# Kernel tuning notes

Hardware: AMD Instinct MI355X
Metric: run time of the kernel (lower is better)

The kernel has to match this reference:

```python
import jax, jax.numpy as jnp
import numpy as np

NAMES = ['tempo', 'chord', 'barbeat', 'type', 'pitch', 'duration', 'velocity']
VOCABS = [56, 135, 18, 4, 87, 18, 25]
EMBS = [128, 256, 64, 32, 512, 128, 128]
B, S, D, H, L, FF = 2, 2048, 512, 8, 8, 2048
HD = D // H
EPS = 1e-6


def _layernorm(x, g, b):
    m = x.mean(-1, keepdims=True)
    v = ((x - m) ** 2).mean(-1, keepdims=True)
    return (x - m) / jnp.sqrt(v + 1e-5) * g + b


def _rope(x, cos, sin):
    x1, x2 = jnp.split(x, 2, -1)
    return x * cos + jnp.concatenate([-x2, x1], -1) * sin


def _causal_linear_attn(q, k, v):
    # kernelized causal linear attention: phi = elu + 1, cumulative-sum normalization
    q = jax.nn.elu(q) + 1.0
    k = jax.nn.elu(k) + 1.0
    kv = jnp.cumsum(jnp.einsum('bshd,bshm->bshdm', k, v), axis=1)  # [B,S,H,HD,HD]
    z = 1.0 / (jnp.einsum('bshd,bshd->bsh', q, jnp.cumsum(k, axis=1)) + EPS)
    return jnp.einsum('bshd,bshdm->bshm', q, kv) * z[..., None]


def _forward(inputs, target, emb_tables, in_W, in_b, Wq, bq, Wk, bk, Wv, bv, Wo, bo,
             ln1_g, ln1_b, ln2_g, ln2_b, W1, b1, W2, b2, norm_g, norm_b, pWs, pbs, catW, catb):
    # multi-field embedding, each scaled by sqrt(d_emb) (CPEmbedding)
    embs = [emb_tables[i][inputs[..., i]] * jnp.sqrt(jnp.float32(EMBS[i])) for i in range(7)]
    x = jnp.concatenate(embs, -1) @ in_W + in_b  # [B,S,D]
    # PositionalEncoding: original indexes pe at position seq_len -> single d_model vector
    div = jnp.exp(jnp.arange(0, D, 2, dtype=jnp.float32) * (-np.log(10000.0) / D))
    pe = jnp.zeros((D,), jnp.float32).at[0::2].set(jnp.sin(S * div)).at[1::2].set(jnp.cos(S * div))
    x = x + pe
    # rotary tables for head_dim
    inv_freq = 1.0 / (10000.0 ** (jnp.arange(0, HD, 2, dtype=jnp.float32) / HD))
    fr = jnp.arange(S, dtype=jnp.float32)[:, None] * inv_freq[None, :]
    ang = jnp.concatenate([fr, fr], -1)  # [S,HD]
    cos = jnp.cos(ang)[None, :, None, :]
    sin = jnp.sin(ang)[None, :, None, :]
    for l in range(L):
        q = (x @ Wq[l] + bq[l]).reshape(B, S, H, HD)
        k = (x @ Wk[l] + bk[l]).reshape(B, S, H, HD)
        v = (x @ Wv[l] + bv[l]).reshape(B, S, H, HD)
        q = _rope(q, cos, sin)
        k = _rope(k, cos, sin)
        a = _causal_linear_attn(q, k, v).reshape(B, S, D) @ Wo[l] + bo[l]
        x = x + a
        y = x = _layernorm(x, ln1_g[l], ln1_b[l])
        y = jax.nn.gelu(y @ W1[l] + b1[l], approximate=False) @ W2[l] + b2[l]
        x = _layernorm(x + y, ln2_g[l], ln2_b[l])
    x = _layernorm(x, norm_g, norm_b)
    # MultiProj with teacher-forced type embedding (target branch)
    emb_t = emb_tables[3][target[..., 3]] * jnp.sqrt(jnp.float32(EMBS[3]))
    proj_type = (x @ pWs[3] + pbs[3]) * jnp.sqrt(jnp.float32(VOCABS[3]))  # from pre-concat x
    xc = jnp.concatenate([x, emb_t], -1) @ catW + catb
    outs = []
    for i in range(7):
        if i == 3:
            outs.append(proj_type)
        else:
            outs.append((xc @ pWs[i] + pbs[i]) * jnp.sqrt(jnp.float32(VOCABS[i])))
    return jnp.concatenate(outs, -1)  # [B,S,sum(VOCABS)=343]


def setup_inputs():
    key = jax.random.key(0)
    kit = iter(jax.random.split(key, 64))
    s = 0.02
    d = {}
    d['inputs'] = jax.random.randint(next(kit), (B, S, 7), 0, 4)
    d['target'] = jax.random.randint(next(kit), (B, S, 7), 0, 4)
    for i, n in enumerate(NAMES):
        d['emb_' + n] = jax.random.normal(next(kit), (VOCABS[i], EMBS[i]), jnp.float32) * s
    E = sum(EMBS)
    d['in_W'] = jax.random.normal(next(kit), (E, D)) * s
    d['in_b'] = jnp.zeros((D,))
    for nm, sh in [('Wq', (L, D, D)), ('Wk', (L, D, D)), ('Wv', (L, D, D)), ('Wo', (L, D, D)), ('W1', (L, D, FF)), ('W2', (L, FF, D))]:
        d[nm] = jax.random.normal(next(kit), sh) * s
    for nm, sh in [('bq', (L, D)), ('bk', (L, D)), ('bv', (L, D)), ('bo', (L, D)), ('b1', (L, FF)), ('b2', (L, D)), ('ln1_b', (L, D)), ('ln2_b', (L, D)), ('norm_b', (D,)), ('catb', (D,))]:
        d[nm] = jnp.zeros(sh)
    d['ln1_g'] = jnp.ones((L, D))
    d['ln2_g'] = jnp.ones((L, D))
    d['norm_g'] = jnp.ones((D,))
    for i, n in enumerate(NAMES):
        d['pW_' + n] = jax.random.normal(next(kit), (D, VOCABS[i])) * s
        d['pb_' + n] = jnp.zeros((VOCABS[i],))
    d['catW'] = jax.random.normal(next(kit), (D + 32, D)) * s
    return d


def reference(inputs, target, emb_tempo, emb_chord, emb_barbeat, emb_type, emb_pitch, emb_duration, emb_velocity,
              in_W, in_b, Wq, bq, Wk, bk, Wv, bv, Wo, bo, ln1_g, ln1_b, ln2_g, ln2_b, W1, b1, W2, b2,
              norm_g, norm_b, pW_tempo, pb_tempo, pW_chord, pb_chord, pW_barbeat, pb_barbeat, pW_type, pb_type,
              pW_pitch, pb_pitch, pW_duration, pb_duration, pW_velocity, pb_velocity, catW, catb):
    emb_tables = [emb_tempo, emb_chord, emb_barbeat, emb_type, emb_pitch, emb_duration, emb_velocity]
    pWs = [pW_tempo, pW_chord, pW_barbeat, pW_type, pW_pitch, pW_duration, pW_velocity]
    pbs = [pb_tempo, pb_chord, pb_barbeat, pb_type, pb_pitch, pb_duration, pb_velocity]
    return _forward(inputs, target, emb_tables, in_W, in_b, Wq, bq, Wk, bk, Wv, bv, Wo, bo,
                    ln1_g, ln1_b, ln2_g, ln2_b, W1, b1, W2, b2, norm_g, norm_b, pWs, pbs, catW, catb)
```

## Files before the change

### kernel.cpp

```cpp
#include <hip/hip_runtime.h>
#include <math.h>

typedef unsigned short u16;
typedef short bf16x8 __attribute__((ext_vector_type(8)));
typedef float f32x4 __attribute__((ext_vector_type(4)));
typedef u16 u16x4 __attribute__((ext_vector_type(4)));
typedef u16 u16x8 __attribute__((ext_vector_type(8)));

#define NB 2
#define NS 2048
#define ND 512
#define NH 8
#define NHD 64
#define NL 8
#define NFF 2048
#define NM (NB*NS)
#define NE 1248
#define NEP 1280
#define NXC 576
#define CHK 64
#define NCH (NS/CHK)
#define QKVW 1536

__device__ inline float b2f(u16 u){ union{ unsigned int i; float f;} x; x.i = ((unsigned int)u)<<16; return x.f; }
__device__ inline u16 f2b(float f){ union{ float f; unsigned int i;} x; x.f=f; unsigned int r = x.i + 0x7fffu + ((x.i>>16)&1u); return (u16)(r>>16); }

__global__ void k_tables(float* rc, float* rs, float* pe){
  int tid = blockIdx.x*blockDim.x + threadIdx.x;
  if (tid < NS*32){
    int s = tid >> 5, j = tid & 31;
    double inv = exp(-(double)(2*j) * log(10000.0) / (double)NHD);
    double ang = (double)s * inv;
    rc[tid] = (float)cos(ang);
    rs[tid] = (float)sin(ang);
  }
  if (tid < ND/2){
    double div = exp(-(double)(2*tid) * log(10000.0) / (double)ND);
    double ang = (double)NS * div;
    pe[2*tid]   = (float)sin(ang);
    pe[2*tid+1] = (float)cos(ang);
  }
}

__global__ void k_embed(const int* __restrict__ inp,
    const float* __restrict__ e0, const float* __restrict__ e1, const float* __restrict__ e2,
    const float* __restrict__ e3, const float* __restrict__ e4, const float* __restrict__ e5,
    const float* __restrict__ e6, u16* __restrict__ xe)
{
  int row = blockIdx.x;
  int i0 = inp[row*7+0], i1 = inp[row*7+1], i2 = inp[row*7+2], i3 = inp[row*7+3],
      i4 = inp[row*7+4], i5 = inp[row*7+5], i6 = inp[row*7+6];
  size_t base = (size_t)row*NEP;
  for (int c = threadIdx.x; c < NEP; c += 256){
    float val = 0.f;
    if      (c < 128)  val = e0[i0*128 + c]        * 11.3137084990f;
    else if (c < 384)  val = e1[i1*256 + (c-128)]  * 16.0f;
    else if (c < 448)  val = e2[i2*64  + (c-384)]  * 8.0f;
    else if (c < 480)  val = e3[i3*32  + (c-448)]  * 5.6568542495f;
    else if (c < 992)  val = e4[i4*512 + (c-480)]  * 22.6274169980f;
    else if (c < 1120) val = e5[i5*128 + (c-992)]  * 11.3137084990f;
    else if (c < NE)   val = e6[i6*128 + (c-1120)] * 11.3137084990f;
    xe[base + c] = f2b(val);
  }
}

__device__ inline void trans_tile(const float* __restrict__ W, u16* __restrict__ WT,
                                  int K, int N, int Kpad, int bx, int by){
  __shared__ float t[32][33];
  int tx = threadIdx.x & 31, ty = threadIdx.x >> 5;
  int k0 = by*32, n0 = bx*32;
  #pragma unroll
  for (int i=0;i<4;i++){
    int k = k0 + ty + i*8, n = n0 + tx;
    t[ty+i*8][tx] = (k<K && n<N) ? W[(size_t)k*N + n] : 0.f;
  }
  __syncthreads();
  #pragma unroll
  for (int i=0;i<4;i++){
    int n = n0 + ty + i*8, k = k0 + tx;
    if (n<N && k<Kpad) WT[(size_t)n*Kpad + k] = f2b(t[tx][ty+i*8]);
  }
}
__global__ void k_trans(const float* __restrict__ W, u16* __restrict__ WT, int K, int N, int Kpad){
  trans_tile(W, WT, K, N, Kpad, blockIdx.x, blockIdx.y);
}
__global__ void k_trans4(const float* __restrict__ Wq, const float* __restrict__ Wk,
                         const float* __restrict__ Wv, const float* __restrict__ Wo,
                         u16* __restrict__ dst){
  int z = blockIdx.z, l = z>>2, s = z&3;
  const float* W = (s==0?Wq:s==1?Wk:s==2?Wv:Wo) + (size_t)l*ND*ND;
  trans_tile(W, dst + (size_t)z*ND*ND, ND, ND, ND, blockIdx.x, blockIdx.y);
}
__global__ void k_transw(const float* __restrict__ W1l, const float* __restrict__ W2l,
                         u16* __restrict__ w1T, u16* __restrict__ w2T){
  int bid = blockIdx.x;
  if (bid < 1024) trans_tile(W1l, w1T, ND, NFF, ND, bid & 63, bid >> 6);
  else { bid -= 1024; trans_tile(W2l, w2T, NFF, ND, NFF, bid & 15, bid >> 4); }
}

template<int ACT, int NT, int TM>
__global__ __launch_bounds__(256) void k_gemm(
    const u16* __restrict__ A, const u16* __restrict__ BT,
    const float* __restrict__ bias, float* __restrict__ Cf, u16* __restrict__ Cb,
    int N, int klen, int lda, int ldb, int ldc,
    int koff, float* __restrict__ Cf2,
    const float* __restrict__ rc, const float* __restrict__ rs)
{
  constexpr int MREP = TM/32;
  __shared__ u16 SH[TM*64 + NT*32*64];
  u16* As = SH;
  u16* Bs = SH + TM*64;
  int tid = threadIdx.x;
  int w = tid >> 6, lane = tid & 63;

  int kz = blockIdx.z;
  A  += (size_t)kz*koff;
  BT += (size_t)kz*koff;
  if (kz){ Cf = Cf2; bias = nullptr; }

  int nwg = gridDim.x*gridDim.y;
  int d = blockIdx.y*gridDim.x + blockIdx.x;
  int wl = ((nwg & 7) == 0) ? ((d & 7)*(nwg >> 3) + (d >> 3)) : d;
  int bx = wl % gridDim.x, by = wl / gridDim.x;
  int m0 = by*TM, n0 = bx*(NT*32);

  f32x4 acc[MREP][NT];
  #pragma unroll
  for (int m=0;m<MREP;m++)
    #pragma unroll
    for (int n=0;n<NT;n++) acc[m][n] = (f32x4){0.f,0.f,0.f,0.f};

  int lg = lane>>3;
  int cg = (lane&7) ^ lg;
  const u16* ag = A  + (size_t)(m0 + w*(TM/4) + lg)*lda + cg*8;
  const u16* bg = BT + (size_t)(n0 + w*(NT*8) + lg)*ldb + cg*8;
  int wr = (w>>1)*(TM/2), wc = (w&1)*(NT*16);
  int lr = lane & 15;
  int rx = lr & 7;
  int cb_ = lane >> 4;
  int g = lane >> 4;

  int nk = klen >> 6;
  for (int t = 0; t < nk; ++t){
    int k0 = t << 6;
    #pragma unroll
    for (int i=0;i<TM/32;i++)
      __builtin_amdgcn_global_load_lds(
        (__attribute__((address_space(1))) void*)(void*)(ag + (size_t)(i*8)*lda + k0),
        (__attribute__((address_space(3))) void*)(&As[(w*(TM/4) + i*8)*64]), 16, 0, 0);
    #pragma unroll
    for (int j=0;j<NT;j++)
      __builtin_amdgcn_global_load_lds(
        (__attribute__((address_space(1))) void*)(void*)(bg + (size_t)(j*8)*ldb + k0),
        (__attribute__((address_space(3))) void*)(&Bs[(w*(NT*8) + j*8)*64]), 16, 0, 0);
    __syncthreads();
    #pragma unroll
    for (int kk=0;kk<2;kk++){
      int gA = ((kk*4 + cb_) ^ rx) * 8;
      bf16x8 af[MREP], bfr[NT];
      #pragma unroll
      for (int m=0;m<MREP;m++) af[m]  = *(const bf16x8*)&As[(wr + m*16 + lr)*64 + gA];
      #pragma unroll
      for (int n=0;n<NT;n++)   bfr[n] = *(const bf16x8*)&Bs[(wc + n*16 + lr)*64 + gA];
      #pragma unroll
      for (int m=0;m<MREP;m++)
        #pragma unroll
        for (int n=0;n<NT;n++)
          acc[m][n] = __builtin_amdgcn_mfma_f32_16x16x32_bf16(af[m], bfr[n], acc[m][n], 0,0,0);
    }
    __syncthreads();
  }

  if (ACT == 2){
    float* Cs = (float*)SH;
    #pragma unroll
    for (int n=0;n<NT;n++){
      int col = wc + n*16 + lr;
      float bv = bias ? bias[n0 + col] : 0.f;
      #pragma unroll
      for (int m=0;m<MREP;m++)
        #pragma unroll
        for (int r=0;r<4;r++)
          Cs[(wr + m*16 + g*4 + r)*64 + col] = acc[m][n][r] + bv;
    }
    __syncthreads();
    if (n0 < 1024){
      #pragma unroll
      for (int i=0;i<8;i++){
        int p = tid + i*256;
        int row = p >> 5, j = p & 31;
        float a1 = Cs[row*64 + j], a2 = Cs[row*64 + j + 32];
        int s = (m0 + row) & (NS-1);
        float c = rc[s*32+j], sn = rs[s*32+j];
        float r1 = a1*c - a2*sn, r2 = a2*c + a1*sn;
        Cb[(size_t)(m0+row)*ldc + n0 + j]      = f2b((r1 > 0.f) ? r1+1.f : expf(r1));
        Cb[(size_t)(m0+row)*ldc + n0 + j + 32] = f2b((r2 > 0.f) ? r2+1.f : expf(r2));
      }
    } else {
      #pragma unroll
      for (int i=0;i<16;i++){
        int p = tid + i*256;
        int row = p >> 6, c2 = p & 63;
        Cb[(size_t)(m0+row)*ldc + n0 + c2] = f2b(Cs[row*64 + c2]);
      }
    }
    return;
  }

  #pragma unroll
  for (int n=0;n<NT;n++){
    int col = n0 + wc + n*16 + lr;
    if (col < N){
      float bv = bias ? bias[col] : 0.f;
      #pragma unroll
      for (int m=0;m<MREP;m++){
        #pragma unroll
        for (int r=0;r<4;r++){
          int row = m0 + wr + m*16 + g*4 + r;
          float v = acc[m][n][r] + bv;
          if (ACT==1) v = 0.5f*v*(1.f+erff(v*0.70710678118654752f));
          if (Cf) Cf[(size_t)row*ldc + col] = v;
          if (Cb) Cb[(size_t)row*ldc + col] = f2b(v);
        }
      }
    }
  }
}

__global__ __launch_bounds__(256) void k_att1(const u16* __restrict__ qkv, float* __restrict__ pref){
  int c = blockIdx.x, h = blockIdx.y, b = blockIdx.z;
  __shared__ u16 Kt[64*64];
  __shared__ u16 Vt[80*64];
  int tid = threadIdx.x;
  {
    int t = tid & 63, dseg = (tid>>6)*16;
    const u16* kg = qkv + ((size_t)(b*NS + c*CHK + t))*QKVW + 512 + h*NHD + dseg;
    u16x8 k0 = *(const u16x8*)kg;
    u16x8 k1 = *(const u16x8*)(kg+8);
    u16x8 v0 = *(const u16x8*)(kg+512);
    u16x8 v1 = *(const u16x8*)(kg+520);
    #pragma unroll
    for (int e=0;e<8;e++){
      int d0 = dseg+e, d1 = dseg+8+e;
      Kt[(d0*64+t) ^ ((d0&7)<<3)] = k0[e];
      Kt[(d1*64+t) ^ ((d1&7)<<3)] = k1[e];
      Vt[(d0*64+t) ^ ((d0&7)<<3)] = v0[e];
      Vt[(d1*64+t) ^ ((d1&7)<<3)] = v1[e];
    }
    if (tid < 64) Vt[4096 + tid] = 0x3F80;
    for (int e = tid; e < 15*64; e += 256){
      int r = 65 + (e>>6), tt = e&63;
      Vt[(r*64+tt) ^ ((r&7)<<3)] = 0;
    }
  }
  __syncthreads();
  int lane = tid & 63, w = tid >> 6;
  int lr = lane & 15, lk = (lane>>4)*8;
  f32x4 acc[5];
  #pragma unroll
  for (int i=0;i<5;i++) acc[i] = (f32x4){0.f,0.f,0.f,0.f};
  #pragma unroll
  for (int kk=0;kk<2;kk++){
    int mcol = w*16 + lr;
    bf16x8 bfrag = *(const bf16x8*)&Kt[(mcol*64 + kk*32 + lk) ^ ((mcol&7)<<3)];
    #pragma unroll
    for (int fr=0; fr<5; fr++){
      int arow = fr*16 + lr;
      bf16x8 afrag = *(const bf16x8*)&Vt[(arow*64 + kk*32 + lk) ^ ((arow&7)<<3)];
      acc[fr] = __builtin_amdgcn_mfma_f32_16x16x32_bf16(afrag, bfrag, acc[fr], 0,0,0);
    }
  }
  size_t base = (((size_t)(b*NH + h))*NCH + c)*5120;
  int g = lane>>4;
  #pragma unroll
  for (int fr=0; fr<5; fr++)
    #pragma unroll
    for (int r=0;r<4;r++)
      pref[base + (fr*16 + g*4 + r)*64 + w*16 + lr] = acc[fr][r];
}

__global__ __launch_bounds__(256) void k_att2(float* __restrict__ pref){
  int bh = blockIdx.y;
  int e = blockIdx.x*256 + threadIdx.x;
  size_t base = (size_t)bh*NCH*5120 + e;
  float v[NCH];
  #pragma unroll
  for (int c=0;c<NCH;c++) v[c] = pref[base + (size_t)c*5120];
  float run = 0.f;
  #pragma unroll
  for (int c=0;c<NCH;c++){ float t = v[c]; pref[base + (size_t)c*5120] = run; run += t; }
}

__global__ __launch_bounds__(256) void k_att3(const u16* __restrict__ qkv,
    const float* __restrict__ pref, u16* __restrict__ outa)
{
  int c = blockIdx.x, h = blockIdx.y, b = blockIdx.z;
  __shared__ u16 Qs[4096], Ks[4096], Sm[4096];
  __shared__ u16 Vt[5120], Ps[5120];
  __shared__ float dens[64];
  int tid = threadIdx.x;
  {
    int row = tid>>2, seg = (tid&3)*16;
    const u16* qg = qkv + ((size_t)(b*NS + c*CHK + row))*QKVW + h*NHD + seg;
    u16x8 q0 = *(const u16x8*)qg;
    u16x8 q1 = *(const u16x8*)(qg+8);
    u16x8 kk0 = *(const u16x8*)(qg+512);
    u16x8 kk1 = *(const u16x8*)(qg+520);
    int sw = (row&7)<<3;
    *(u16x8*)&Qs[(row*64+seg) ^ sw]     = q0;
    *(u16x8*)&Qs[(row*64+seg+8) ^ sw]   = q1;
    *(u16x8*)&Ks[(row*64+seg) ^ sw]     = kk0;
    *(u16x8*)&Ks[(row*64+seg+8) ^ sw]   = kk1;
  }
  {
    int t = tid&63, dseg = (tid>>6)*16;
    const u16* vg = qkv + ((size_t)(b*NS + c*CHK + t))*QKVW + 1024 + h*NHD + dseg;
    u16x8 v0 = *(const u16x8*)vg;
    u16x8 v1 = *(const u16x8*)(vg+8);
    #pragma unroll
    for (int e=0;e<8;e++){
      int d0=dseg+e, d1=dseg+8+e;
      Vt[(d0*64+t)^((d0&7)<<3)] = v0[e];
      Vt[(d1*64+t)^((d1&7)<<3)] = v1[e];
    }
    if (tid<64) Vt[4096+tid] = 0x3F80;
    for (int e=tid; e<15*64; e+=256){
      int r = 65+(e>>6), tt = e&63;
      Vt[(r*64+tt)^((r&7)<<3)] = 0;
    }
  }
  {
    size_t pb = (((size_t)(b*NH + h))*NCH + c)*5120;
    for (int e=tid; e<5120; e+=256){
      int row = e>>6, m = e&63;
      Ps[(row*64+m)^((row&7)<<3)] = f2b(pref[pb+e]);
    }
  }
  __syncthreads();
  int lane = tid&63, w = tid>>6;
  int lr = lane&15, lk = (lane>>4)*8, g = lane>>4;
  f32x4 sacc[4];
  #pragma unroll
  for (int i=0;i<4;i++) sacc[i] = (f32x4){0.f,0.f,0.f,0.f};
  int iq = w*16 + lr;
  #pragma unroll
  for (int kk=0;kk<2;kk++){
    bf16x8 bq = *(const bf16x8*)&Qs[(iq*64 + kk*32 + lk) ^ ((iq&7)<<3)];
    #pragma unroll
    for (int ft=0; ft<4; ft++){
      int tr = ft*16 + lr;
      bf16x8 ak = *(const bf16x8*)&Ks[(tr*64 + kk*32 + lk) ^ ((tr&7)<<3)];
      sacc[ft] = __builtin_amdgcn_mfma_f32_16x16x32_bf16(ak, bq, sacc[ft], 0,0,0);
    }
  }
  #pragma unroll
  for (int ft=0; ft<4; ft++){
    int t0 = ft*16 + g*4;
    u16x4 pk;
    #pragma unroll
    for (int r=0;r<4;r++) pk[r] = f2b((t0+r <= iq) ? sacc[ft][r] : 0.f);
    *(u16x4*)&Sm[(iq*64 + t0) ^ ((iq&7)<<3)] = pk;
  }
  __syncthreads();
  f32x4 acc[5];
  #pragma unroll
  for (int i=0;i<5;i++) acc[i] = (f32x4){0.f,0.f,0.f,0.f};
  #pragma unroll
  for (int kk=0;kk<2;kk++){
    int sw = (iq&7)<<3;
    bf16x8 as = *(const bf16x8*)&Sm[(iq*64 + kk*32 + lk) ^ sw];
    bf16x8 aq = *(const bf16x8*)&Qs[(iq*64 + kk*32 + lk) ^ sw];
    #pragma unroll
    for (int c5=0;c5<5;c5++){
      int col = c5*16 + lr, sw2 = (col&7)<<3;
      bf16x8 bv = *(const bf16x8*)&Vt[(col*64 + kk*32 + lk) ^ sw2];
      bf16x8 bp = *(const bf16x8*)&Ps[(col*64 + kk*32 + lk) ^ sw2];
      acc[c5] = __builtin_amdgcn_mfma_f32_16x16x32_bf16(as, bv, acc[c5], 0,0,0);
      acc[c5] = __builtin_amdgcn_mfma_f32_16x16x32_bf16(aq, bp, acc[c5], 0,0,0);
    }
  }
  if (lr == 0){
    #pragma unroll
    for (int r=0;r<4;r++) dens[w*16 + g*4 + r] = acc[4][r];
  }
  __syncthreads();
  #pragma unroll
  for (int c5=0;c5<4;c5++){
    #pragma unroll
    for (int r=0;r<4;r++){
      int i = w*16 + g*4 + r;
      float z = 1.f/(dens[i] + 1e-6f);
      outa[((size_t)(b*NS + c*CHK + i))*ND + h*NHD + c5*16 + lr] = f2b(acc[c5][r]*z);
    }
  }
}

__global__ __launch_bounds__(256) void k_ln(const float* __restrict__ xin, const float* __restrict__ res,
    const float* __restrict__ res2, float* __restrict__ outx, u16* __restrict__ outb,
    const float* __restrict__ g, const float* __restrict__ bvec)
{
  int row = blockIdx.x, tid = threadIdx.x;
  size_t base = (size_t)row*ND;
  float v0 = xin[base+tid], v1 = xin[base+tid+256];
  if (res){ v0 += res[base+tid]; v1 += res[base+tid+256]; }
  if (res2){ v0 += res2[base+tid]; v1 += res2[base+tid+256]; }
  float s = v0+v1, ss2 = v0*v0 + v1*v1;
  #pragma unroll
  for (int o = 32; o >= 1; o >>= 1){
    s   += __shfl_down(s, o, 64);
    ss2 += __shfl_down(ss2, o, 64);
  }
  __shared__ float red[8];
  int wv = tid >> 6, ln = tid & 63;
  if (ln == 0){ red[wv] = s; red[4+wv] = ss2; }
  __syncthreads();
  float stot  = red[0]+red[1]+red[2]+red[3];
  float sstot = red[4]+red[5]+red[6]+red[7];
  float mean = stot * (1.0f/ND);
  float var  = sstot * (1.0f/ND) - mean*mean;
  float inv = 1.0f / sqrtf(var + 1e-5f);
  float o0 = (v0-mean)*inv*g[tid]     + bvec[tid];
  float o1 = (v1-mean)*inv*g[tid+256] + bvec[tid+256];
  outx[base+tid] = o0; outx[base+tid+256] = o1;
  if (outb){ outb[base+tid] = f2b(o0); outb[base+tid+256] = f2b(o1); }
}

__global__ void k_xc(const float* __restrict__ x, const int* __restrict__ tgt,
                     const float* __restrict__ embt, u16* __restrict__ xc){
  int row = blockIdx.x;
  int id = tgt[row*7+3];
  size_t base = (size_t)row*NXC;
  for (int c = threadIdx.x; c < NXC; c += 256){
    float v = (c < ND) ? x[(size_t)row*ND + c]
            : (c < 544 ? embt[id*32 + (c-ND)]*5.6568542495f : 0.f);
    xc[base + c] = f2b(v);
  }
}

__global__ void k_pack(const float* p0,const float* p1,const float* p2,const float* p3,
                       const float* p4,const float* p5,const float* p6,
                       const float* q0,const float* q1,const float* q2,const float* q3,
                       const float* q4,const float* q5,const float* q6,
                       u16* __restrict__ pwcT, float* __restrict__ pbc,
                       u16* __restrict__ ptT, float* __restrict__ pbt){
  int idx = blockIdx.x*256 + threadIdx.x;
  const int off[8] = {0,56,191,209,213,300,318,343};
  int col = idx >> 9, k = idx & 511;
  if (col < 384){
    u16 v = 0;
    if (col < 343){
      int f = 0;
      while (col >= off[f+1]) f++;
      int cc = col - off[f];
      int V = off[f+1]-off[f];
      const float* P = (f==0)?p0:(f==1)?p1:(f==2)?p2:(f==3)?p3:(f==4)?p4:(f==5)?p5:p6;
      v = f2b(P[(size_t)k*V + cc] * sqrtf((float)V));
    }
    pwcT[(size_t)col*512 + k] = v;
  }
  if (idx < 64*512){
    int n = idx >> 9;
    ptT[idx] = (n < 4) ? f2b(p3[(size_t)k*4 + n]*2.0f) : (u16)0;
  }
  if (idx < 343){
    int c2 = idx, f = 0;
    while (c2 >= off[f+1]) f++;
    int cc = c2 - off[f]; int V = off[f+1]-off[f];
    const float* Q = (f==0)?q0:(f==1)?q1:(f==2)?q2:(f==3)?q3:(f==4)?q4:(f==5)?q5:q6;
    pbc[idx] = Q[cc]*sqrtf((float)V);
  }
  if (idx < 4) pbt[idx] = q3[idx]*2.0f;
}

__global__ void k_bqkv(const float* __restrict__ bq, const float* __restrict__ bk,
                       const float* __restrict__ bv, float* __restrict__ dst,
                       const float* __restrict__ in_b, const float* __restrict__ pe,
                       float* __restrict__ bias_in){
  int idx = blockIdx.x*256 + threadIdx.x;
  if (idx < NL*QKVW){
    int l = idx / QKVW, c = idx % QKVW;
    float v = (c < 512) ? bq[l*512 + c] : (c < 1024) ? bk[l*512 + c - 512] : bv[l*512 + c - 1024];
    dst[idx] = v;
  }
  if (idx < ND) bias_in[idx] = in_b[idx] + pe[idx];
}

extern "C" void kernel_launch(void* const* d_in, const int* in_sizes, int n_in,
                              void* d_out, int out_size, void* d_ws, size_t ws_size,
                              hipStream_t stream)
{
  const int* inputs = (const int*)d_in[0];
  const int* target = (const int*)d_in[1];
  const float* emb[7];
  for (int i=0;i<7;i++) emb[i] = (const float*)d_in[2+i];
  const float* in_W  = (const float*)d_in[9];
  const float* in_b  = (const float*)d_in[10];
  const float* Wq = (const float*)d_in[11];
  const float* Wk = (const float*)d_in[12];
  const float* Wv = (const float*)d_in[13];
  const float* Wo = (const float*)d_in[14];
  const float* W1 = (const float*)d_in[15];
  const float* W2 = (const float*)d_in[16];
  const float* bq = (const float*)d_in[17];
  const float* bk = (const float*)d_in[18];
  const float* bv = (const float*)d_in[19];
  const float* bo = (const float*)d_in[20];
  const float* b1 = (const float*)d_in[21];
  const float* b2 = (const float*)d_in[22];
  const float* ln1_b = (const float*)d_in[23];
  const float* ln2_b = (const float*)d_in[24];
  const float* norm_b = (const float*)d_in[25];
  const float* catb   = (const float*)d_in[26];
  const float* ln1_g = (const float*)d_in[27];
  const float* ln2_g = (const float*)d_in[28];
  const float* norm_g = (const float*)d_in[29];
  const float* pW[7]; const float* pb[7];
  for (int i=0;i<7;i++){ pW[i]=(const float*)d_in[30+2*i]; pb[i]=(const float*)d_in[31+2*i]; }
  const float* catW = (const float*)d_in[44];
  float* outp = (float*)d_out;

  char* base = (char*)d_ws;
  size_t off = 0;
  auto alloc = [&](size_t bytes)->void*{ void* p = base + off; off += bytes; off = (off + 255) & ~(size_t)255; return p; };

  float* x    = (float*)alloc((size_t)NM*ND*4);
  u16*   xb   = (u16*)  alloc((size_t)NM*ND*2);
  u16*   qkvb = (u16*)  alloc((size_t)NM*QKVW*2);
  float* tb   = (float*)alloc((size_t)NM*ND*4);
  float* tb2  = (float*)alloc((size_t)NM*ND*4);
  u16*   ab   = (u16*)  alloc((size_t)NM*ND*2);
  u16*   hb   = (u16*)  alloc((size_t)NM*NFF*2);
  float* rc   = (float*)alloc((size_t)NS*32*4);
  float* rs   = (float*)alloc((size_t)NS*32*4);
  float* pe   = (float*)alloc(ND*4);
  float* pref = (float*)alloc((size_t)NB*NH*NCH*5120*4);
  u16*  qkvoT = (u16*)  alloc((size_t)NL*4*ND*ND*2);
  u16*  w1T   = (u16*)  alloc((size_t)NFF*ND*2);
  u16*  w2T   = (u16*)  alloc((size_t)ND*NFF*2);
  u16*  inWT  = (u16*)  alloc((size_t)ND*NEP*2);
  u16*  catWT = (u16*)  alloc((size_t)ND*NXC*2);
  u16*  pwcT  = (u16*)  alloc((size_t)384*512*2);
  float* pbc  = (float*)alloc(344*4);
  u16*  ptT   = (u16*)  alloc((size_t)64*512*2);
  float* pbt  = (float*)alloc(4*4);
  float* bqkv = (float*)alloc((size_t)NL*QKVW*4);
  float* bias_in = (float*)alloc(ND*4);
  u16*  xeb = hb;
  u16*  xcb = hb;
  u16*  ocb = hb + (size_t)NM*NXC;

  k_tables<<<256, 256, 0, stream>>>(rc, rs, pe);
  k_trans4<<<dim3(16,16,32), 256, 0, stream>>>(Wq, Wk, Wv, Wo, qkvoT);
  k_trans<<<dim3(16,40), 256, 0, stream>>>(in_W, inWT, NE, ND, NEP);
  k_trans<<<dim3(16,18), 256, 0, stream>>>(catW, catWT, 544, ND, NXC);
  k_pack<<<768, 256, 0, stream>>>(pW[0],pW[1],pW[2],pW[3],pW[4],pW[5],pW[6],
                                  pb[0],pb[1],pb[2],pb[3],pb[4],pb[5],pb[6],
                                  pwcT, pbc, ptT, pbt);
  k_bqkv<<<(NL*QKVW+255)/256, 256, 0, stream>>>(bq, bk, bv, bqkv, in_b, pe, bias_in);

  k_embed<<<NM, 256, 0, stream>>>(inputs, emb[0],emb[1],emb[2],emb[3],emb[4],emb[5],emb[6], xeb);
  k_gemm<0,2,64><<<dim3(8,64,1), 256, 0, stream>>>(xeb, inWT, bias_in, x, xb,
      ND, NEP, NEP, NEP, ND, 0, nullptr, nullptr, nullptr);

  dim3 agrid(NCH, NH, NB);
  for (int l = 0; l < NL; l++){
    k_transw<<<2048, 256, 0, stream>>>(W1 + (size_t)l*ND*NFF, W2 + (size_t)l*NFF*ND, w1T, w2T);
    const u16* woT = qkvoT + (size_t)(l*4+3)*ND*ND;
    k_gemm<2,2,64><<<dim3(24,64,1), 256, 0, stream>>>(xb, qkvoT + (size_t)l*4*ND*ND,
        bqkv + l*QKVW, nullptr, qkvb, QKVW, ND, ND, ND, QKVW, 0, nullptr, rc, rs);
    k_att1<<<agrid, 256, 0, stream>>>(qkvb, pref);
    k_att2<<<dim3(20,16), 256, 0, stream>>>(pref);
    k_att3<<<agrid, 256, 0, stream>>>(qkvb, pref, ab);
    k_gemm<0,2,64><<<dim3(8,64,2), 256, 0, stream>>>(ab, woT, bo + l*ND, tb, nullptr,
        ND, 256, ND, ND, ND, 256, tb2, nullptr, nullptr);
    k_ln<<<NM, 256, 0, stream>>>(x, tb, tb2, x, xb, ln1_g + l*ND, ln1_b + l*ND);
    k_gemm<1,2,64><<<dim3(32,64,1), 256, 0, stream>>>(xb, w1T, b1 + l*NFF, nullptr, hb,
        NFF, ND, ND, ND, NFF, 0, nullptr, nullptr, nullptr);
    k_gemm<0,2,64><<<dim3(8,64,2), 256, 0, stream>>>(hb, w2T, b2 + l*ND, tb, nullptr,
        ND, 1024, NFF, NFF, ND, 1024, tb2, nullptr, nullptr);
    k_ln<<<NM, 256, 0, stream>>>(x, tb, tb2, x, xb, ln2_g + l*ND, ln2_b + l*ND);
  }

  k_ln<<<NM, 256, 0, stream>>>(x, nullptr, nullptr, x, xb, norm_g, norm_b);

  k_xc<<<NM, 256, 0, stream>>>(x, target, emb[3], xcb);
  k_gemm<0,2,64><<<dim3(8,64,1), 256, 0, stream>>>(xcb, catWT, catb, nullptr, ocb,
      ND, NXC, NXC, NXC, ND, 0, nullptr, nullptr, nullptr);
  k_gemm<0,2,64><<<dim3(6,64,1), 256, 0, stream>>>(ocb, pwcT, pbc, outp, nullptr,
      343, ND, ND, ND, 343, 0, nullptr, nullptr, nullptr);
  k_gemm<0,2,64><<<dim3(1,64,1), 256, 0, stream>>>(xb, ptT, pbt, outp + 209, nullptr,
      4, ND, ND, ND, 343, 0, nullptr, nullptr, nullptr);
}
```

Baseline: 861.9 us.

## Merge weight prep into one launch, fuse xc build into final layernorm

All weight transposes, including every layer's W1/W2, are now done up front in a single large kernel, and the small table, pack and bias kernels are merged into one. This removes one launch per layer plus several setup launches. The final layernorm now also writes the concatenated cat-input buffer, which removes the separate k_xc pass. In attention phase 3 the score matrix reuses the K shared buffer, with an extra barrier, to cut LDS use. The cost is eight times more scratch memory for the transposed FFN weights.

```diff
diff --git a/kernel.cpp b/kernel.cpp
--- a/kernel.cpp
+++ b/kernel.cpp
@@ -25,23 +25,6 @@
 __device__ inline float b2f(u16 u){ union{ unsigned int i; float f;} x; x.i = ((unsigned int)u)<<16; return x.f; }
 __device__ inline u16 f2b(float f){ union{ float f; unsigned int i;} x; x.f=f; unsigned int r = x.i + 0x7fffu + ((x.i>>16)&1u); return (u16)(r>>16); }
 
-__global__ void k_tables(float* rc, float* rs, float* pe){
-  int tid = blockIdx.x*blockDim.x + threadIdx.x;
-  if (tid < NS*32){
-    int s = tid >> 5, j = tid & 31;
-    double inv = exp(-(double)(2*j) * log(10000.0) / (double)NHD);
-    double ang = (double)s * inv;
-    rc[tid] = (float)cos(ang);
-    rs[tid] = (float)sin(ang);
-  }
-  if (tid < ND/2){
-    double div = exp(-(double)(2*tid) * log(10000.0) / (double)ND);
-    double ang = (double)NS * div;
-    pe[2*tid]   = (float)sin(ang);
-    pe[2*tid+1] = (float)cos(ang);
-  }
-}
-
 __global__ void k_embed(const int* __restrict__ inp,
     const float* __restrict__ e0, const float* __restrict__ e1, const float* __restrict__ e2,
     const float* __restrict__ e3, const float* __restrict__ e4, const float* __restrict__ e5,
@@ -81,21 +64,91 @@
     if (n<N && k<Kpad) WT[(size_t)n*Kpad + k] = f2b(t[tx][ty+i*8]);
   }
 }
-__global__ void k_trans(const float* __restrict__ W, u16* __restrict__ WT, int K, int N, int Kpad){
-  trans_tile(W, WT, K, N, Kpad, blockIdx.x, blockIdx.y);
-}
-__global__ void k_trans4(const float* __restrict__ Wq, const float* __restrict__ Wk,
-                         const float* __restrict__ Wv, const float* __restrict__ Wo,
-                         u16* __restrict__ dst){
-  int z = blockIdx.z, l = z>>2, s = z&3;
-  const float* W = (s==0?Wq:s==1?Wk:s==2?Wv:Wo) + (size_t)l*ND*ND;
-  trans_tile(W, dst + (size_t)z*ND*ND, ND, ND, ND, blockIdx.x, blockIdx.y);
-}
-__global__ void k_transw(const float* __restrict__ W1l, const float* __restrict__ W2l,
-                         u16* __restrict__ w1T, u16* __restrict__ w2T){
+
+__global__ void k_prepw(const float* __restrict__ Wq, const float* __restrict__ Wk,
+                        const float* __restrict__ Wv, const float* __restrict__ Wo,
+                        const float* __restrict__ in_W, const float* __restrict__ catW,
+                        const float* __restrict__ W1, const float* __restrict__ W2,
+                        u16* __restrict__ qkvoT, u16* __restrict__ inWT, u16* __restrict__ catWT,
+                        u16* __restrict__ w1T, u16* __restrict__ w2T)
+{
   int bid = blockIdx.x;
-  if (bid < 1024) trans_tile(W1l, w1T, ND, NFF, ND, bid & 63, bid >> 6);
-  else { bid -= 1024; trans_tile(W2l, w2T, NFF, ND, NFF, bid & 15, bid >> 4); }
+  if (bid < 8192){
+    int z = bid >> 8, r = bid & 255;
+    int l = z >> 2, s2 = z & 3;
+    const float* W = (s2==0?Wq:s2==1?Wk:s2==2?Wv:Wo) + (size_t)l*ND*ND;
+    trans_tile(W, qkvoT + (size_t)z*ND*ND, ND, ND, ND, r & 15, r >> 4);
+  } else if (bid < 8832){
+    int r = bid - 8192;
+    trans_tile(in_W, inWT, NE, ND, NEP, r & 15, r >> 4);
+  } else if (bid < 9120){
+    int r = bid - 8832;
+    trans_tile(catW, catWT, 544, ND, NXC, r & 15, r >> 4);
+  } else {
+    int r = bid - 9120;
+    int l = r >> 11; int b2 = r & 2047;
+    if (b2 < 1024) trans_tile(W1 + (size_t)l*ND*NFF, w1T + (size_t)l*ND*NFF, ND, NFF, ND, b2 & 63, b2 >> 6);
+    else { b2 -= 1024; trans_tile(W2 + (size_t)l*NFF*ND, w2T + (size_t)l*NFF*ND, NFF, ND, NFF, b2 & 15, b2 >> 4); }
+  }
+}
+
+__global__ void k_misc(float* __restrict__ rc, float* __restrict__ rs,
+    const float* p0,const float* p1,const float* p2,const float* p3,
+    const float* p4,const float* p5,const float* p6,
+    const float* q0,const float* q1,const float* q2,const float* q3,
+    const float* q4,const float* q5,const float* q6,
+    u16* __restrict__ pwcT, float* __restrict__ pbc,
+    u16* __restrict__ ptT, float* __restrict__ pbt,
+    const float* __restrict__ bq, const float* __restrict__ bk, const float* __restrict__ bv,
+    float* __restrict__ bqkv, const float* __restrict__ in_b, float* __restrict__ bias_in)
+{
+  int idx = blockIdx.x*256 + threadIdx.x;
+  if (idx < NS*32){
+    int s = idx >> 5, j = idx & 31;
+    double inv = exp(-(double)(2*j) * log(10000.0) / (double)NHD);
+    double ang = (double)s * inv;
+    rc[idx] = (float)cos(ang);
+    rs[idx] = (float)sin(ang);
+  }
+  const int off[8] = {0,56,191,209,213,300,318,343};
+  {
+    int col = idx >> 9, k = idx & 511;
+    if (col < 384){
+      u16 v = 0;
+      if (col < 343){
+        int f = 0;
+        while (col >= off[f+1]) f++;
+        int cc = col - off[f];
+        int V = off[f+1]-off[f];
+        const float* P = (f==0)?p0:(f==1)?p1:(f==2)?p2:(f==3)?p3:(f==4)?p4:(f==5)?p5:p6;
+        v = f2b(P[(size_t)k*V + cc] * sqrtf((float)V));
+      }
+      pwcT[(size_t)col*512 + k] = v;
+    }
+    if (idx < 64*512){
+      int n = idx >> 9;
+      ptT[idx] = (n < 4) ? f2b(p3[(size_t)k*4 + n]*2.0f) : (u16)0;
+    }
+  }
+  if (idx < 343){
+    int c2 = idx, f = 0;
+    while (c2 >= off[f+1]) f++;
+    int cc = c2 - off[f]; int V = off[f+1]-off[f];
+    const float* Q = (f==0)?q0:(f==1)?q1:(f==2)?q2:(f==3)?q3:(f==4)?q4:(f==5)?q5:q6;
+    pbc[idx] = Q[cc]*sqrtf((float)V);
+  }
+  if (idx < 4) pbt[idx] = q3[idx]*2.0f;
+  if (idx < NL*QKVW){
+    int l = idx / QKVW, c = idx % QKVW;
+    float v = (c < 512) ? bq[l*512 + c] : (c < 1024) ? bk[l*512 + c - 512] : bv[l*512 + c - 1024];
+    bqkv[idx] = v;
+  }
+  if (idx < ND){
+    double div = exp(-(double)(idx & ~1) * log(10000.0) / (double)ND);
+    double ang = (double)NS * div;
+    float pev = (idx & 1) ? (float)cos(ang) : (float)sin(ang);
+    bias_in[idx] = in_b[idx] + pev;
+  }
 }
 
 template<int ACT, int NT, int TM>
@@ -295,9 +348,10 @@
     const float* __restrict__ pref, u16* __restrict__ outa)
 {
   int c = blockIdx.x, h = blockIdx.y, b = blockIdx.z;
-  __shared__ u16 Qs[4096], Ks[4096], Sm[4096];
+  __shared__ u16 Qs[4096], Ks[4096];
   __shared__ u16 Vt[5120], Ps[5120];
   __shared__ float dens[64];
+  u16* Sm = Ks;
   int tid = threadIdx.x;
   {
     int row = tid>>2, seg = (tid&3)*16;
@@ -353,6 +407,7 @@
       sacc[ft] = __builtin_amdgcn_mfma_f32_16x16x32_bf16(ak, bq, sacc[ft], 0,0,0);
     }
   }
+  __syncthreads();
   #pragma unroll
   for (int ft=0; ft<4; ft++){
     int t0 = ft*16 + g*4;
@@ -397,7 +452,8 @@
 
 __global__ __launch_bounds__(256) void k_ln(const float* __restrict__ xin, const float* __restrict__ res,
     const float* __restrict__ res2, float* __restrict__ outx, u16* __restrict__ outb,
-    const float* __restrict__ g, const float* __restrict__ bvec)
+    const float* __restrict__ g, const float* __restrict__ bvec,
+    const int* __restrict__ tgt, const float* __restrict__ embt, u16* __restrict__ xcb)
 {
   int row = blockIdx.x, tid = threadIdx.x;
   size_t base = (size_t)row*ND;
@@ -423,66 +479,16 @@
   float o1 = (v1-mean)*inv*g[tid+256] + bvec[tid+256];
   outx[base+tid] = o0; outx[base+tid+256] = o1;
   if (outb){ outb[base+tid] = f2b(o0); outb[base+tid+256] = f2b(o1); }
-}
-
-__global__ void k_xc(const float* __restrict__ x, const int* __restrict__ tgt,
-                     const float* __restrict__ embt, u16* __restrict__ xc){
-  int row = blockIdx.x;
-  int id = tgt[row*7+3];
-  size_t base = (size_t)row*NXC;
-  for (int c = threadIdx.x; c < NXC; c += 256){
-    float v = (c < ND) ? x[(size_t)row*ND + c]
-            : (c < 544 ? embt[id*32 + (c-ND)]*5.6568542495f : 0.f);
-    xc[base + c] = f2b(v);
-  }
-}
-
-__global__ void k_pack(const float* p0,const float* p1,const float* p2,const float* p3,
-                       const float* p4,const float* p5,const float* p6,
-                       const float* q0,const float* q1,const float* q2,const float* q3,
-                       const float* q4,const float* q5,const float* q6,
-                       u16* __restrict__ pwcT, float* __restrict__ pbc,
-                       u16* __restrict__ ptT, float* __restrict__ pbt){
-  int idx = blockIdx.x*256 + threadIdx.x;
-  const int off[8] = {0,56,191,209,213,300,318,343};
-  int col = idx >> 9, k = idx & 511;
-  if (col < 384){
-    u16 v = 0;
-    if (col < 343){
-      int f = 0;
-      while (col >= off[f+1]) f++;
-      int cc = col - off[f];
-      int V = off[f+1]-off[f];
-      const float* P = (f==0)?p0:(f==1)?p1:(f==2)?p2:(f==3)?p3:(f==4)?p4:(f==5)?p5:p6;
-      v = f2b(P[(size_t)k*V + cc] * sqrtf((float)V));
-    }
-    pwcT[(size_t)col*512 + k] = v;
-  }
-  if (idx < 64*512){
-    int n = idx >> 9;
-    ptT[idx] = (n < 4) ? f2b(p3[(size_t)k*4 + n]*2.0f) : (u16)0;
-  }
-  if (idx < 343){
-    int c2 = idx, f = 0;
-    while (c2 >= off[f+1]) f++;
-    int cc = c2 - off[f]; int V = off[f+1]-off[f];
-    const float* Q = (f==0)?q0:(f==1)?q1:(f==2)?q2:(f==3)?q3:(f==4)?q4:(f==5)?q5:q6;
-    pbc[idx] = Q[cc]*sqrtf((float)V);
-  }
-  if (idx < 4) pbt[idx] = q3[idx]*2.0f;
-}
-
-__global__ void k_bqkv(const float* __restrict__ bq, const float* __restrict__ bk,
-                       const float* __restrict__ bv, float* __restrict__ dst,
-                       const float* __restrict__ in_b, const float* __restrict__ pe,
-                       float* __restrict__ bias_in){
-  int idx = blockIdx.x*256 + threadIdx.x;
-  if (idx < NL*QKVW){
-    int l = idx / QKVW, c = idx % QKVW;
-    float v = (c < 512) ? bq[l*512 + c] : (c < 1024) ? bk[l*512 + c - 512] : bv[l*512 + c - 1024];
-    dst[idx] = v;
-  }
-  if (idx < ND) bias_in[idx] = in_b[idx] + pe[idx];
+  if (xcb){
+    size_t xbse = (size_t)row*NXC;
+    xcb[xbse+tid] = f2b(o0);
+    xcb[xbse+tid+256] = f2b(o1);
+    if (tid < 32){
+      int id = tgt[row*7+3];
+      xcb[xbse+512+tid] = f2b(embt[id*32+tid]*5.6568542495f);
+      xcb[xbse+544+tid] = 0;
+    }
+  }
 }
 
 extern "C" void kernel_launch(void* const* d_in, const int* in_sizes, int n_in,
@@ -532,11 +538,10 @@
   u16*   hb   = (u16*)  alloc((size_t)NM*NFF*2);
   float* rc   = (float*)alloc((size_t)NS*32*4);
   float* rs   = (float*)alloc((size_t)NS*32*4);
-  float* pe   = (float*)alloc(ND*4);
   float* pref = (float*)alloc((size_t)NB*NH*NCH*5120*4);
   u16*  qkvoT = (u16*)  alloc((size_t)NL*4*ND*ND*2);
-  u16*  w1T   = (u16*)  alloc((size_t)NFF*ND*2);
-  u16*  w2T   = (u16*)  alloc((size_t)ND*NFF*2);
+  u16*  w1T   = (u16*)  alloc((size_t)NL*NFF*ND*2);
+  u16*  w2T   = (u16*)  alloc((size_t)NL*ND*NFF*2);
   u16*  inWT  = (u16*)  alloc((size_t)ND*NEP*2);
   u16*  catWT = (u16*)  alloc((size_t)ND*NXC*2);
   u16*  pwcT  = (u16*)  alloc((size_t)384*512*2);
@@ -549,14 +554,12 @@
   u16*  xcb = hb;
   u16*  ocb = hb + (size_t)NM*NXC;
 
-  k_tables<<<256, 256, 0, stream>>>(rc, rs, pe);
-  k_trans4<<<dim3(16,16,32), 256, 0, stream>>>(Wq, Wk, Wv, Wo, qkvoT);
-  k_trans<<<dim3(16,40), 256, 0, stream>>>(in_W, inWT, NE, ND, NEP);
-  k_trans<<<dim3(16,18), 256, 0, stream>>>(catW, catWT, 544, ND, NXC);
-  k_pack<<<768, 256, 0, stream>>>(pW[0],pW[1],pW[2],pW[3],pW[4],pW[5],pW[6],
-                                  pb[0],pb[1],pb[2],pb[3],pb[4],pb[5],pb[6],
-                                  pwcT, pbc, ptT, pbt);
-  k_bqkv<<<(NL*QKVW+255)/256, 256, 0, stream>>>(bq, bk, bv, bqkv, in_b, pe, bias_in);
+  k_prepw<<<25504, 256, 0, stream>>>(Wq, Wk, Wv, Wo, in_W, catW, W1, W2,
+                                     qkvoT, inWT, catWT, w1T, w2T);
+  k_misc<<<768, 256, 0, stream>>>(rc, rs,
+      pW[0],pW[1],pW[2],pW[3],pW[4],pW[5],pW[6],
+      pb[0],pb[1],pb[2],pb[3],pb[4],pb[5],pb[6],
+      pwcT, pbc, ptT, pbt, bq, bk, bv, bqkv, in_b, bias_in);
 
   k_embed<<<NM, 256, 0, stream>>>(inputs, emb[0],emb[1],emb[2],emb[3],emb[4],emb[5],emb[6], xeb);
   k_gemm<0,2,64><<<dim3(8,64,1), 256, 0, stream>>>(xeb, inWT, bias_in, x, xb,
@@ -564,7 +567,6 @@
 
   dim3 agrid(NCH, NH, NB);
   for (int l = 0; l < NL; l++){
-    k_transw<<<2048, 256, 0, stream>>>(W1 + (size_t)l*ND*NFF, W2 + (size_t)l*NFF*ND, w1T, w2T);
     const u16* woT = qkvoT + (size_t)(l*4+3)*ND*ND;
     k_gemm<2,2,64><<<dim3(24,64,1), 256, 0, stream>>>(xb, qkvoT + (size_t)l*4*ND*ND,
         bqkv + l*QKVW, nullptr, qkvb, QKVW, ND, ND, ND, QKVW, 0, nullptr, rc, rs);
@@ -573,17 +575,19 @@
     k_att3<<<agrid, 256, 0, stream>>>(qkvb, pref, ab);
     k_gemm<0,2,64><<<dim3(8,64,2), 256, 0, stream>>>(ab, woT, bo + l*ND, tb, nullptr,
         ND, 256, ND, ND, ND, 256, tb2, nullptr, nullptr);
-    k_ln<<<NM, 256, 0, stream>>>(x, tb, tb2, x, xb, ln1_g + l*ND, ln1_b + l*ND);
-    k_gemm<1,2,64><<<dim3(32,64,1), 256, 0, stream>>>(xb, w1T, b1 + l*NFF, nullptr, hb,
-        NFF, ND, ND, ND, NFF, 0, nullptr, nullptr, nullptr);
-    k_gemm<0,2,64><<<dim3(8,64,2), 256, 0, stream>>>(hb, w2T, b2 + l*ND, tb, nullptr,
-        ND, 1024, NFF, NFF, ND, 1024, tb2, nullptr, nullptr);
-    k_ln<<<NM, 256, 0, stream>>>(x, tb, tb2, x, xb, ln2_g + l*ND, ln2_b + l*ND);
-  }
-
-  k_ln<<<NM, 256, 0, stream>>>(x, nullptr, nullptr, x, xb, norm_g, norm_b);
-
-  k_xc<<<NM, 256, 0, stream>>>(x, target, emb[3], xcb);
+    k_ln<<<NM, 256, 0, stream>>>(x, tb, tb2, x, xb, ln1_g + l*ND, ln1_b + l*ND,
+                                 nullptr, nullptr, nullptr);
+    k_gemm<1,2,64><<<dim3(32,64,1), 256, 0, stream>>>(xb, w1T + (size_t)l*NFF*ND,
+        b1 + l*NFF, nullptr, hb, NFF, ND, ND, ND, NFF, 0, nullptr, nullptr, nullptr);
+    k_gemm<0,2,64><<<dim3(8,64,2), 256, 0, stream>>>(hb, w2T + (size_t)l*ND*NFF,
+        b2 + l*ND, tb, nullptr, ND, 1024, NFF, NFF, ND, 1024, tb2, nullptr, nullptr);
+    k_ln<<<NM, 256, 0, stream>>>(x, tb, tb2, x, xb, ln2_g + l*ND, ln2_b + l*ND,
+                                 nullptr, nullptr, nullptr);
+  }
+
+  k_ln<<<NM, 256, 0, stream>>>(x, nullptr, nullptr, x, xb, norm_g, norm_b,
+                               target, emb[3], xcb);
+
   k_gemm<0,2,64><<<dim3(8,64,1), 256, 0, stream>>>(xcb, catWT, catb, nullptr, ocb,
       ND, NXC, NXC, NXC, ND, 0, nullptr, nullptr, nullptr);
   k_gemm<0,2,64><<<dim3(6,64,1), 256, 0, stream>>>(ocb, pwcT, pbc, outp, nullptr,
```

Result: faster. 828.5 us (-3.9%).
